# Kernel optimization log

Hardware: AMD Instinct MI355X
Metric: run time of the kernel (lower is better)

The kernel has to match this reference:

```python
import jax, jax.numpy as jnp
import numpy as np
from jax import lax

INPUT_SIZE, HIDDEN, NUM_LAYERS, NUM_CLASSES = 22, 10, 2, 4
B, T = 1024, 1000


def _run_layer(seq, w_ih, w_hh, b_ih, b_hh):
    # seq: (T, B, F_in) -> (T, B, H); Elman RNN with ReLU nonlinearity
    h0 = jnp.zeros((seq.shape[1], w_hh.shape[0]), seq.dtype)
    def step(h, x_t):
        h_new = jax.nn.relu(x_t @ w_ih.T + h @ w_hh.T + (b_ih + b_hh))
        return h_new, h_new
    _, hs = lax.scan(step, h0, seq)
    return hs


def setup_inputs() -> dict:
    key = jax.random.key(0)
    ks = jax.random.split(key, 12)
    s = 1.0 / np.sqrt(HIDDEN)  # torch nn.RNN init scale
    u = lambda k, shape: jax.random.uniform(k, shape, jnp.float32, -s, s)
    return {
        "x": jax.random.normal(ks[0], (B, T, INPUT_SIZE), jnp.float32),
        "w_ih0": u(ks[1], (HIDDEN, INPUT_SIZE)),
        "w_hh0": u(ks[2], (HIDDEN, HIDDEN)),
        "b_ih0": u(ks[3], (HIDDEN,)),
        "b_hh0": u(ks[4], (HIDDEN,)),
        "w_ih1": u(ks[5], (HIDDEN, HIDDEN)),
        "w_hh1": u(ks[6], (HIDDEN, HIDDEN)),
        "b_ih1": u(ks[7], (HIDDEN,)),
        "b_hh1": u(ks[8], (HIDDEN,)),
        "w_lin": u(ks[9], (NUM_CLASSES, HIDDEN)),
        "b_lin": u(ks[10], (NUM_CLASSES,)),
    }


def reference(x, w_ih0, w_hh0, b_ih0, b_hh0, w_ih1, w_hh1, b_ih1, b_hh1, w_lin, b_lin):
    seq = jnp.transpose(x, (1, 0, 2))                      # (T, B, F)
    h1 = _run_layer(seq, w_ih0, w_hh0, b_ih0, b_hh0)       # (T, B, H)
    h2 = _run_layer(h1, w_ih1, w_hh1, b_ih1, b_hh1)        # (T, B, H)
    last = jax.nn.relu(h2[-1])                             # (B, H)
    return last @ w_lin.T + b_lin                          # (B, num_classes)
```

## Files before the change

kernel.cpp:

```cpp
#include <hip/hip_runtime.h>

typedef float v2f __attribute__((ext_vector_type(2)));

namespace {

constexpr int Tn = 1000, Fn = 22, Hn = 10, Cn = 4;
constexpr int ROWB = Tn * Fn * 4;
constexpr int CHF  = 32 * Fn;
constexpr int CHB  = CHF * 4;

__device__ __forceinline__ v2f mk2(float a, float b) { v2f r; r.x=a; r.y=b; return r; }
__device__ __forceinline__ v2f fma2(v2f a, v2f b, v2f c) { return __builtin_elementwise_fma(a,b,c); }
__device__ __forceinline__ float rlane(float v, int l) {
    return __uint_as_float(__builtin_amdgcn_readlane(__float_as_uint(v), l));
}
__device__ __forceinline__ void gld_lds4(const float* g, float* l) {
    __builtin_amdgcn_global_load_lds(
        (const __attribute__((address_space(1))) unsigned int*)g,
        (__attribute__((address_space(3))) unsigned int*)l, 4, 0, 0);
}
__device__ __forceinline__ void sfence() { __builtin_amdgcn_sched_barrier(0); }

__global__ __launch_bounds__(64, 1) void rnn_fat2(
    const float* __restrict__ x,
    const float* __restrict__ w_ih0, const float* __restrict__ w_hh0,
    const float* __restrict__ b_ih0, const float* __restrict__ b_hh0,
    const float* __restrict__ w_ih1, const float* __restrict__ w_hh1,
    const float* __restrict__ b_ih1, const float* __restrict__ b_hh1,
    const float* __restrict__ w_lin, const float* __restrict__ b_lin,
    float* __restrict__ out)
{
    __shared__ __align__(16) float ch[2][CHF];

    const int lane = threadIdx.x;
    const int b    = blockIdx.x;
    const int half = lane >> 5;
    const int l31  = lane & 31;

    const int jz = (l31 < Hn) ? l31 : 0;
    const bool isl2 = (l31 >= 16) && (l31 < 16 + Hn);
    const int j2 = isl2 ? (l31 - 16) : 0;

    const float* pwa = (l31 < 16) ? (w_hh0 + jz * Hn) : (w_ih1 + j2 * Hn);
    float wa[Hn], wb[Hn];
    #pragma unroll
    for (int k = 0; k < Hn; ++k) wa[k] = pwa[k];
    #pragma unroll
    for (int k = 0; k < Hn; ++k) wb[k] = isl2 ? w_hh1[j2 * Hn + k] : 0.f;
    v2f wih0p[11];
    #pragma unroll
    for (int p = 0; p < 11; ++p)
        wih0p[p] = mk2(w_ih0[jz * Fn + 2*p], w_ih0[jz * Fn + 2*p + 1]);
    const float bias1  = b_ih0[jz] + b_hh0[jz];
    const float bias2v = b_ih1[j2] + b_hh1[j2];
    const v2f bz2 = mk2(bias1, 0.f);

    const bool mL = (lane < Hn);
    const bool mU = (lane >= 32) && (lane < 32+Hn);

    const float* __restrict__ xrow = x + (size_t)b * (Tn * Fn);

    auto stage = [&](int c) {
        float* dst = ch[c & 1];
        const float* src = xrow + c * CHF;
        if (c < 31) {
            #pragma unroll
            for (int k = 0; k < 11; ++k) gld_lds4(src + k*64 + lane, dst + k*64);
        } else {
            gld_lds4(src + lane, dst);
            gld_lds4(src + 64 + lane, dst + 64);
            if (lane < 48) gld_lds4(src + 128 + lane, dst + 128);
        }
    };
    stage(0); stage(1);

    v2f xd[11], xv0[11], xv1[11];
    {
        const float* r01 = xrow + half * Fn;
        #pragma unroll
        for (int p = 0; p < 11; ++p) xd[p] = ((const v2f*)r01)[p];
        const float* r23 = xrow + (2 + half) * Fn;
        #pragma unroll
        for (int p = 0; p < 11; ++p) xv0[p] = ((const v2f*)r23)[p];
    }

    auto zc = [&](const v2f* xp) -> float {
        v2f z = fma2(xp[0], wih0p[0], bz2);
        #pragma unroll
        for (int p = 1; p < 11; ++p) z = fma2(xp[p], wih0p[p], z);
        return z.x + z.y;
    };

    auto pairptr = [&](int P) -> const float* {
        return &ch[(P >> 4) & 1][(P & 15) * 44 + half * 22];
    };
    auto loadxv = [&](v2f* dst, const float* rp) {
        #pragma unroll
        for (int p = 0; p < 11; ++p) dst[p] = ((const v2f*)rp)[p];
        sfence();
    };

    float S1[Hn], S2[Hn];
    #pragma unroll
    for (int k = 0; k < Hn; ++k) { S1[k] = 0.f; S2[k] = 0.f; }

    asm volatile("s_waitcnt vmcnt(0)" ::: "memory");
    float zA = zc(xd);
    float zB;

    auto dostep = [&](bool up, float z, bool commit2) {
        const float base = (up ? mU : mL) ? z : bias2v;
        float a = fmaf(S1[0], wa[0], base);
        float c = S1[1] * wa[1];
        a = fmaf(S1[2], wa[2], a);  c = fmaf(S1[3], wa[3], c);
        a = fmaf(S1[4], wa[4], a);  c = fmaf(S1[5], wa[5], c);
        a = fmaf(S1[6], wa[6], a);  c = fmaf(S1[7], wa[7], c);
        a = fmaf(S1[8], wa[8], a);  c = fmaf(S1[9], wa[9], c);
        a = fmaf(S2[0], wb[0], a);  c = fmaf(S2[1], wb[1], c);
        a = fmaf(S2[2], wb[2], a);  c = fmaf(S2[3], wb[3], c);
        a = fmaf(S2[4], wb[4], a);  c = fmaf(S2[5], wb[5], c);
        a = fmaf(S2[6], wb[6], a);  c = fmaf(S2[7], wb[7], c);
        a = fmaf(S2[8], wb[8], a);  c = fmaf(S2[9], wb[9], c);
        const float hn = fmaxf(a + c, 0.f);
        if (!up) {
            #pragma unroll
            for (int k = 0; k < Hn; ++k) S1[k] = rlane(hn, k);
            if (commit2) {
                #pragma unroll
                for (int k = 0; k < Hn; ++k) S2[k] = rlane(hn, 16 + k);
            }
        } else {
            #pragma unroll
            for (int k = 0; k < Hn; ++k) S1[k] = rlane(hn, 32 + k);
            if (commit2) {
                #pragma unroll
                for (int k = 0; k < Hn; ++k) S2[k] = rlane(hn, 48 + k);
            }
        }
    };

    auto MACRO = [&](int m, bool s2_0, bool ld0, bool ld1, bool z1) {
        if (ld0) loadxv(xv1, pairptr(2*m + 2));
        dostep(false, zA, s2_0);
        zB = zc(xv0);
        dostep(true, zA, true);
        if (ld1) loadxv(xv0, pairptr(2*m + 3));
        dostep(false, zB, true);
        if (z1) zA = zc(xv1);
        dostep(true, zB, true);
    };

    MACRO(0, false, true, true, true);

    #pragma unroll 1
    for (int m = 1; m < 249; ++m) {
        if ((m & 7) == 7) {
            asm volatile("s_waitcnt vmcnt(0)" ::: "memory");
            const int c = (m >> 3) + 2;
            if (c <= 31) stage(c);
        }
        MACRO(m, true, true, true, true);
    }
    MACRO(249, true, false, false, false);

    {
        float a = fmaf(S1[0], wa[0], bias2v);
        float c = S1[1] * wa[1];
        a = fmaf(S1[2], wa[2], a);  c = fmaf(S1[3], wa[3], c);
        a = fmaf(S1[4], wa[4], a);  c = fmaf(S1[5], wa[5], c);
        a = fmaf(S1[6], wa[6], a);  c = fmaf(S1[7], wa[7], c);
        a = fmaf(S1[8], wa[8], a);  c = fmaf(S1[9], wa[9], c);
        a = fmaf(S2[0], wb[0], a);  c = fmaf(S2[1], wb[1], c);
        a = fmaf(S2[2], wb[2], a);  c = fmaf(S2[3], wb[3], c);
        a = fmaf(S2[4], wb[4], a);  c = fmaf(S2[5], wb[5], c);
        a = fmaf(S2[6], wb[6], a);  c = fmaf(S2[7], wb[7], c);
        a = fmaf(S2[8], wb[8], a);  c = fmaf(S2[9], wb[9], c);
        const float hn = fmaxf(a + c, 0.f);
        #pragma unroll
        for (int k = 0; k < Hn; ++k) S2[k] = rlane(hn, 16 + k);
    }

    const int jc = (lane < Cn) ? lane : 0;
    float o = b_lin[jc];
    #pragma unroll
    for (int k = 0; k < Hn; ++k) o = fmaf(S2[k], w_lin[jc * Hn + k], o);
    if (lane < Cn) out[b * Cn + lane] = o;
}

}

extern "C" void kernel_launch(void* const* d_in, const int* in_sizes, int n_in,
                              void* d_out, int out_size, void* d_ws, size_t ws_size,
                              hipStream_t stream) {
    const float* x     = (const float*)d_in[0];
    const float* w_ih0 = (const float*)d_in[1];
    const float* w_hh0 = (const float*)d_in[2];
    const float* b_ih0 = (const float*)d_in[3];
    const float* b_hh0 = (const float*)d_in[4];
    const float* w_ih1 = (const float*)d_in[5];
    const float* w_hh1 = (const float*)d_in[6];
    const float* b_ih1 = (const float*)d_in[7];
    const float* b_hh1 = (const float*)d_in[8];
    const float* w_lin = (const float*)d_in[9];
    const float* b_lin = (const float*)d_in[10];
    float* out = (float*)d_out;

    rnn_fat2<<<dim3(1024), dim3(64), 0, stream>>>(
        x, w_ih0, w_hh0, b_ih0, b_hh0,
        w_ih1, w_hh1, b_ih1, b_hh1, w_lin, b_lin, out);
}
```

Baseline: 116.7 us.

## Split RNN layers across two wavefronts with an LDS ring pipeline

Replaces the single-wave kernel, which computed both layers in one interleaved dependency chain, with a two-wave block. Wave 0 runs layer 0 and writes hidden states into a double-buffered LDS ring. Wave 1 consumes them 32 timesteps behind to run layer 1 and the final linear layer. Each wave now has a shorter serial chain per step (10 FMAs instead of 20 for layer 0), at the cost of LDS traffic, a block barrier every 32 steps, and twice as many waves per CU.

```diff
diff --git a/kernel.cpp b/kernel.cpp
--- a/kernel.cpp
+++ b/kernel.cpp
@@ -5,9 +5,9 @@
 namespace {
 
 constexpr int Tn = 1000, Fn = 22, Hn = 10, Cn = 4;
-constexpr int ROWB = Tn * Fn * 4;
-constexpr int CHF  = 32 * Fn;
-constexpr int CHB  = CHF * 4;
+constexpr int CHF   = 32 * Fn;
+constexpr int RINGF = 2 * CHF;
+constexpr int LDSF  = RINGF + 2 * 32 * 16;
 
 __device__ __forceinline__ v2f mk2(float a, float b) { v2f r; r.x=a; r.y=b; return r; }
 __device__ __forceinline__ v2f fma2(v2f a, v2f b, v2f c) { return __builtin_elementwise_fma(a,b,c); }
@@ -20,8 +20,12 @@
         (__attribute__((address_space(3))) unsigned int*)l, 4, 0, 0);
 }
 __device__ __forceinline__ void sfence() { __builtin_amdgcn_sched_barrier(0); }
-
-__global__ __launch_bounds__(64, 1) void rnn_fat2(
+__device__ __forceinline__ void lgkm0_bar() {
+    asm volatile("s_waitcnt lgkmcnt(0)" ::: "memory");
+    __builtin_amdgcn_s_barrier();
+}
+
+__global__ __launch_bounds__(128, 2) void rnn_pipe(
     const float* __restrict__ x,
     const float* __restrict__ w_ih0, const float* __restrict__ w_hh0,
     const float* __restrict__ b_ih0, const float* __restrict__ b_hh0,
@@ -30,161 +34,202 @@
     const float* __restrict__ w_lin, const float* __restrict__ b_lin,
     float* __restrict__ out)
 {
-    __shared__ __align__(16) float ch[2][CHF];
-
-    const int lane = threadIdx.x;
+    __shared__ __align__(16) float lds[LDSF];
+    float* xch  = lds;
+    float* ring = lds + RINGF;
+
+    const int tid  = threadIdx.x;
+    const int wid  = tid >> 6;
+    const int lane = tid & 63;
     const int b    = blockIdx.x;
-    const int half = lane >> 5;
-    const int l31  = lane & 31;
-
-    const int jz = (l31 < Hn) ? l31 : 0;
-    const bool isl2 = (l31 >= 16) && (l31 < 16 + Hn);
-    const int j2 = isl2 ? (l31 - 16) : 0;
-
-    const float* pwa = (l31 < 16) ? (w_hh0 + jz * Hn) : (w_ih1 + j2 * Hn);
-    float wa[Hn], wb[Hn];
-    #pragma unroll
-    for (int k = 0; k < Hn; ++k) wa[k] = pwa[k];
-    #pragma unroll
-    for (int k = 0; k < Hn; ++k) wb[k] = isl2 ? w_hh1[j2 * Hn + k] : 0.f;
-    v2f wih0p[11];
-    #pragma unroll
-    for (int p = 0; p < 11; ++p)
-        wih0p[p] = mk2(w_ih0[jz * Fn + 2*p], w_ih0[jz * Fn + 2*p + 1]);
-    const float bias1  = b_ih0[jz] + b_hh0[jz];
-    const float bias2v = b_ih1[j2] + b_hh1[j2];
-    const v2f bz2 = mk2(bias1, 0.f);
-
-    const bool mL = (lane < Hn);
-    const bool mU = (lane >= 32) && (lane < 32+Hn);
-
     const float* __restrict__ xrow = x + (size_t)b * (Tn * Fn);
 
-    auto stage = [&](int c) {
-        float* dst = ch[c & 1];
-        const float* src = xrow + c * CHF;
-        if (c < 31) {
-            #pragma unroll
-            for (int k = 0; k < 11; ++k) gld_lds4(src + k*64 + lane, dst + k*64);
-        } else {
-            gld_lds4(src + lane, dst);
-            gld_lds4(src + 64 + lane, dst + 64);
-            if (lane < 48) gld_lds4(src + 128 + lane, dst + 128);
+    if (wid == 0) {
+        const int half = lane >> 5;
+        const int l31  = lane & 31;
+        const int jz   = (l31 < Hn) ? l31 : 0;
+
+        v2f wih0p[11];
+        #pragma unroll
+        for (int p = 0; p < 11; ++p)
+            wih0p[p] = mk2(w_ih0[jz*Fn + 2*p], w_ih0[jz*Fn + 2*p + 1]);
+        float wa[Hn];
+        #pragma unroll
+        for (int k = 0; k < Hn; ++k) wa[k] = w_hh0[jz*Hn + k];
+        const v2f bz2 = mk2(b_ih0[jz] + b_hh0[jz], 0.f);
+
+        const int jslotE = (lane < 10) ? lane : 10;
+        const int jslotO = (lane >= 32 && lane < 42) ? (lane - 32) : 11;
+
+        auto stage = [&](int c) {
+            float* dst = xch + (c & 1) * CHF;
+            const float* src = xrow + c * CHF;
+            if (c < 31) {
+                #pragma unroll
+                for (int k = 0; k < 11; ++k) gld_lds4(src + k*64 + lane, dst + k*64);
+            } else {
+                gld_lds4(src + lane, dst);
+                gld_lds4(src + 64 + lane, dst + 64);
+                if (lane < 48) gld_lds4(src + 128 + lane, dst + 128);
+            }
+        };
+
+        v2f xv0[11], xv1[11];
+        float S1[Hn];
+        #pragma unroll
+        for (int k = 0; k < Hn; ++k) S1[k] = 0.f;
+
+        auto zc = [&](const v2f* xp) -> float {
+            v2f z = fma2(xp[0], wih0p[0], bz2);
+            #pragma unroll
+            for (int p = 1; p < 11; ++p) z = fma2(xp[p], wih0p[p], z);
+            return z.x + z.y;
+        };
+        auto loadxv = [&](v2f* dst, const float* rp) {
+            #pragma unroll
+            for (int p = 0; p < 11; ++p) dst[p] = *(const v2f*)(rp + 2*p);
+            sfence();
+        };
+
+        float zA, zB;
+        auto aStep = [&](bool up, float z, float* wptr, int foff) {
+            float a = fmaf(S1[0], wa[0], z);
+            float c = S1[1]*wa[1];
+            a = fmaf(S1[2],wa[2],a);  c = fmaf(S1[3],wa[3],c);
+            a = fmaf(S1[4],wa[4],a);  c = fmaf(S1[5],wa[5],c);
+            a = fmaf(S1[6],wa[6],a);  c = fmaf(S1[7],wa[7],c);
+            a = fmaf(S1[8],wa[8],a);  c = fmaf(S1[9],wa[9],c);
+            const float hn = fmaxf(a + c, 0.f);
+            const int base = up ? 32 : 0;
+            #pragma unroll
+            for (int k = 0; k < Hn; ++k) S1[k] = rlane(hn, base + k);
+            wptr[foff] = hn;
+        };
+        auto aMacro = [&](const float* xb_t, const float* xb_n, int mm,
+                          float* wE, float* wO, bool ld0, bool ld1, bool z1) {
+            const float* l0 = (mm < 7) ? xb_t + (2*mm + 2)*44 : xb_n;
+            const float* l1 = (mm < 7) ? xb_t + (2*mm + 3)*44 : xb_n + 44;
+            if (ld0) loadxv(xv1, l0);
+            aStep(false, zA, wE, mm*64);
+            zB = zc(xv0);
+            aStep(true,  zA, wO, mm*64 + 16);
+            if (ld1) loadxv(xv0, l1);
+            aStep(false, zB, wE, mm*64 + 32);
+            if (z1) zA = zc(xv1);
+            aStep(true,  zB, wO, mm*64 + 48);
+        };
+
+        stage(0); stage(1);
+        {
+            v2f xd[11];
+            const float* r01 = xrow + half * Fn;
+            #pragma unroll
+            for (int p = 0; p < 11; ++p) xd[p] = *(const v2f*)(r01 + 2*p);
+            const float* r23 = xrow + (2 + half) * Fn;
+            #pragma unroll
+            for (int p = 0; p < 11; ++p) xv0[p] = *(const v2f*)(r23 + 2*p);
+            asm volatile("s_waitcnt vmcnt(0)" ::: "memory");
+            zA = zc(xd);
         }
-    };
-    stage(0); stage(1);
-
-    v2f xd[11], xv0[11], xv1[11];
-    {
-        const float* r01 = xrow + half * Fn;
-        #pragma unroll
-        for (int p = 0; p < 11; ++p) xd[p] = ((const v2f*)r01)[p];
-        const float* r23 = xrow + (2 + half) * Fn;
-        #pragma unroll
-        for (int p = 0; p < 11; ++p) xv0[p] = ((const v2f*)r23)[p];
+
+        #pragma unroll 1
+        for (int p = 0; p <= 32; ++p) {
+            if (p <= 30) {
+                const int xs = p & 1;
+                const float* xb_t = xch + xs*CHF + half*22;
+                const float* xb_n = xch + (xs^1)*CHF + half*22;
+                float* wE = ring + xs*512 + jslotE;
+                float* wO = ring + xs*512 + jslotO;
+                #pragma unroll
+                for (int mm = 0; mm < 7; ++mm)
+                    aMacro(xb_t, xb_n, mm, wE, wO, true, true, true);
+                asm volatile("s_waitcnt vmcnt(0)" ::: "memory");
+                if (p <= 29) stage(p + 2);
+                aMacro(xb_t, xb_n, 7, wE, wO, true, true, true);
+            } else if (p == 31) {
+                const float* xb_t = xch + CHF + half*22;
+                const float* xb_n = xch + half*22;
+                float* wE = ring + 512 + jslotE;
+                float* wO = ring + 512 + jslotO;
+                aMacro(xb_t, xb_n, 0, wE, wO, true, true, true);
+                aMacro(xb_t, xb_n, 1, wE, wO, false, false, false);
+            }
+            lgkm0_bar();
+        }
+    } else {
+        const int j2 = (lane < Hn) ? lane : 0;
+        v2f wih1p[5];
+        #pragma unroll
+        for (int p = 0; p < 5; ++p)
+            wih1p[p] = mk2(w_ih1[j2*Hn + 2*p], w_ih1[j2*Hn + 2*p + 1]);
+        float whh1r[Hn];
+        #pragma unroll
+        for (int k = 0; k < Hn; ++k) whh1r[k] = w_hh1[j2*Hn + k];
+        const v2f b2v = mk2(b_ih1[j2] + b_hh1[j2], 0.f);
+        const int jc = (lane < Cn) ? lane : 0;
+        float wl[Hn];
+        #pragma unroll
+        for (int k = 0; k < Hn; ++k) wl[k] = w_lin[jc*Hn + k];
+        const float blv = b_lin[jc];
+
+        float S2[Hn];
+        #pragma unroll
+        for (int k = 0; k < Hn; ++k) S2[k] = 0.f;
+        v2f hv0[5], hv1[5];
+
+        auto bload = [&](v2f* d, const float* rp) {
+            #pragma unroll
+            for (int k = 0; k < 5; ++k) d[k] = *(const v2f*)(rp + 2*k);
+            sfence();
+        };
+        auto bStep = [&](const v2f* hp) {
+            v2f acc = fma2(hp[0], wih1p[0], b2v);
+            acc = fma2(hp[1], wih1p[1], acc);
+            acc = fma2(hp[2], wih1p[2], acc);
+            acc = fma2(hp[3], wih1p[3], acc);
+            acc = fma2(hp[4], wih1p[4], acc);
+            float d = acc.x + acc.y;
+            d = fmaf(S2[0],whh1r[0],d);  d = fmaf(S2[1],whh1r[1],d);
+            d = fmaf(S2[2],whh1r[2],d);  d = fmaf(S2[3],whh1r[3],d);
+            d = fmaf(S2[4],whh1r[4],d);  d = fmaf(S2[5],whh1r[5],d);
+            d = fmaf(S2[6],whh1r[6],d);  d = fmaf(S2[7],whh1r[7],d);
+            d = fmaf(S2[8],whh1r[8],d);  d = fmaf(S2[9],whh1r[9],d);
+            const float hn = fmaxf(d, 0.f);
+            #pragma unroll
+            for (int k = 0; k < Hn; ++k) S2[k] = rlane(hn, k);
+        };
+
+        #pragma unroll 1
+        for (int p = 0; p <= 32; ++p) {
+            if (p >= 1) {
+                const float* rb = ring + ((p-1) & 1) * 512;
+                bload(hv0, rb);
+                if (p < 32) {
+                    #pragma unroll
+                    for (int s = 0; s < 32; ++s) {
+                        v2f* cur = (s & 1) ? hv1 : hv0;
+                        v2f* nxt = (s & 1) ? hv0 : hv1;
+                        if (s + 1 < 32) bload(nxt, rb + (s+1)*16);
+                        bStep(cur);
+                    }
+                } else {
+                    #pragma unroll
+                    for (int s = 0; s < 8; ++s) {
+                        v2f* cur = (s & 1) ? hv1 : hv0;
+                        v2f* nxt = (s & 1) ? hv0 : hv1;
+                        if (s + 1 < 8) bload(nxt, rb + (s+1)*16);
+                        bStep(cur);
+                    }
+                }
+            }
+            lgkm0_bar();
+        }
+
+        float o = blv;
+        #pragma unroll
+        for (int k = 0; k < Hn; ++k) o = fmaf(S2[k], wl[k], o);
+        if (lane < Cn) out[b * Cn + lane] = o;
     }
-
-    auto zc = [&](const v2f* xp) -> float {
-        v2f z = fma2(xp[0], wih0p[0], bz2);
-        #pragma unroll
-        for (int p = 1; p < 11; ++p) z = fma2(xp[p], wih0p[p], z);
-        return z.x + z.y;
-    };
-
-    auto pairptr = [&](int P) -> const float* {
-        return &ch[(P >> 4) & 1][(P & 15) * 44 + half * 22];
-    };
-    auto loadxv = [&](v2f* dst, const float* rp) {
-        #pragma unroll
-        for (int p = 0; p < 11; ++p) dst[p] = ((const v2f*)rp)[p];
-        sfence();
-    };
-
-    float S1[Hn], S2[Hn];
-    #pragma unroll
-    for (int k = 0; k < Hn; ++k) { S1[k] = 0.f; S2[k] = 0.f; }
-
-    asm volatile("s_waitcnt vmcnt(0)" ::: "memory");
-    float zA = zc(xd);
-    float zB;
-
-    auto dostep = [&](bool up, float z, bool commit2) {
-        const float base = (up ? mU : mL) ? z : bias2v;
-        float a = fmaf(S1[0], wa[0], base);
-        float c = S1[1] * wa[1];
-        a = fmaf(S1[2], wa[2], a);  c = fmaf(S1[3], wa[3], c);
-        a = fmaf(S1[4], wa[4], a);  c = fmaf(S1[5], wa[5], c);
-        a = fmaf(S1[6], wa[6], a);  c = fmaf(S1[7], wa[7], c);
-        a = fmaf(S1[8], wa[8], a);  c = fmaf(S1[9], wa[9], c);
-        a = fmaf(S2[0], wb[0], a);  c = fmaf(S2[1], wb[1], c);
-        a = fmaf(S2[2], wb[2], a);  c = fmaf(S2[3], wb[3], c);
-        a = fmaf(S2[4], wb[4], a);  c = fmaf(S2[5], wb[5], c);
-        a = fmaf(S2[6], wb[6], a);  c = fmaf(S2[7], wb[7], c);
-        a = fmaf(S2[8], wb[8], a);  c = fmaf(S2[9], wb[9], c);
-        const float hn = fmaxf(a + c, 0.f);
-        if (!up) {
-            #pragma unroll
-            for (int k = 0; k < Hn; ++k) S1[k] = rlane(hn, k);
-            if (commit2) {
-                #pragma unroll
-                for (int k = 0; k < Hn; ++k) S2[k] = rlane(hn, 16 + k);
-            }
-        } else {
-            #pragma unroll
-            for (int k = 0; k < Hn; ++k) S1[k] = rlane(hn, 32 + k);
-            if (commit2) {
-                #pragma unroll
-                for (int k = 0; k < Hn; ++k) S2[k] = rlane(hn, 48 + k);
-            }
-        }
-    };
-
-    auto MACRO = [&](int m, bool s2_0, bool ld0, bool ld1, bool z1) {
-        if (ld0) loadxv(xv1, pairptr(2*m + 2));
-        dostep(false, zA, s2_0);
-        zB = zc(xv0);
-        dostep(true, zA, true);
-        if (ld1) loadxv(xv0, pairptr(2*m + 3));
-        dostep(false, zB, true);
-        if (z1) zA = zc(xv1);
-        dostep(true, zB, true);
-    };
-
-    MACRO(0, false, true, true, true);
-
-    #pragma unroll 1
-    for (int m = 1; m < 249; ++m) {
-        if ((m & 7) == 7) {
-            asm volatile("s_waitcnt vmcnt(0)" ::: "memory");
-            const int c = (m >> 3) + 2;
-            if (c <= 31) stage(c);
-        }
-        MACRO(m, true, true, true, true);
-    }
-    MACRO(249, true, false, false, false);
-
-    {
-        float a = fmaf(S1[0], wa[0], bias2v);
-        float c = S1[1] * wa[1];
-        a = fmaf(S1[2], wa[2], a);  c = fmaf(S1[3], wa[3], c);
-        a = fmaf(S1[4], wa[4], a);  c = fmaf(S1[5], wa[5], c);
-        a = fmaf(S1[6], wa[6], a);  c = fmaf(S1[7], wa[7], c);
-        a = fmaf(S1[8], wa[8], a);  c = fmaf(S1[9], wa[9], c);
-        a = fmaf(S2[0], wb[0], a);  c = fmaf(S2[1], wb[1], c);
-        a = fmaf(S2[2], wb[2], a);  c = fmaf(S2[3], wb[3], c);
-        a = fmaf(S2[4], wb[4], a);  c = fmaf(S2[5], wb[5], c);
-        a = fmaf(S2[6], wb[6], a);  c = fmaf(S2[7], wb[7], c);
-        a = fmaf(S2[8], wb[8], a);  c = fmaf(S2[9], wb[9], c);
-        const float hn = fmaxf(a + c, 0.f);
-        #pragma unroll
-        for (int k = 0; k < Hn; ++k) S2[k] = rlane(hn, 16 + k);
-    }
-
-    const int jc = (lane < Cn) ? lane : 0;
-    float o = b_lin[jc];
-    #pragma unroll
-    for (int k = 0; k < Hn; ++k) o = fmaf(S2[k], w_lin[jc * Hn + k], o);
-    if (lane < Cn) out[b * Cn + lane] = o;
 }
 
 }
@@ -205,7 +250,7 @@
     const float* b_lin = (const float*)d_in[10];
     float* out = (float*)d_out;
 
-    rnn_fat2<<<dim3(1024), dim3(64), 0, stream>>>(
+    rnn_pipe<<<dim3(1024), dim3(128), 0, stream>>>(
         x, w_ih0, w_hh0, b_ih0, b_hh0,
         w_ih1, w_hh1, b_ih1, b_hh1, w_lin, b_lin, out);
 }
```

Result: slower. 137.3 us (+17.6%).

## Exchange hidden state through LDS broadcast instead of readlane

Applied to the files above, without the earlier changes.

Replaces the per-step v_readlane broadcast of the hidden state, which took 20 scalar readlanes per step, with writes of each lane's output into a small LDS scratch area followed by broadcast v2f reads. The recurrent dot products now use packed v2f FMAs with split accumulators for layer 1 and layer 2. The aim is to shorten the serial per-timestep critical path. The trade-off is LDS write-to-read latency on every step, and it depends on ordering within a single wave without explicit waits.

```diff
diff --git a/kernel.cpp b/kernel.cpp
--- a/kernel.cpp
+++ b/kernel.cpp
@@ -5,23 +5,24 @@
 namespace {
 
 constexpr int Tn = 1000, Fn = 22, Hn = 10, Cn = 4;
-constexpr int ROWB = Tn * Fn * 4;
 constexpr int CHF  = 32 * Fn;
-constexpr int CHB  = CHF * 4;
-
-__device__ __forceinline__ v2f mk2(float a, float b) { v2f r; r.x=a; r.y=b; return r; }
-__device__ __forceinline__ v2f fma2(v2f a, v2f b, v2f c) { return __builtin_elementwise_fma(a,b,c); }
-__device__ __forceinline__ float rlane(float v, int l) {
+constexpr int HB   = 2 * CHF;
+constexpr int LDSF = HB + 128;
+
+__device__ __forceinline__ v2f mk2(float a, float b){ v2f r; r.x=a; r.y=b; return r; }
+__device__ __forceinline__ v2f fma2(v2f a, v2f b, v2f c){ return __builtin_elementwise_fma(a,b,c); }
+__device__ __forceinline__ float rlane(float v, int l){
     return __uint_as_float(__builtin_amdgcn_readlane(__float_as_uint(v), l));
 }
-__device__ __forceinline__ void gld_lds4(const float* g, float* l) {
+__device__ __forceinline__ void gld_lds4(const float* g, float* l){
     __builtin_amdgcn_global_load_lds(
         (const __attribute__((address_space(1))) unsigned int*)g,
         (__attribute__((address_space(3))) unsigned int*)l, 4, 0, 0);
 }
-__device__ __forceinline__ void sfence() { __builtin_amdgcn_sched_barrier(0); }
-
-__global__ __launch_bounds__(64, 1) void rnn_fat2(
+__device__ __forceinline__ void sfence(){ __builtin_amdgcn_sched_barrier(0); }
+
+
+__global__ __launch_bounds__(64, 1) void rnn_lds(
     const float* __restrict__ x,
     const float* __restrict__ w_ih0, const float* __restrict__ w_hh0,
     const float* __restrict__ b_ih0, const float* __restrict__ b_hh0,
@@ -30,38 +31,40 @@
     const float* __restrict__ w_lin, const float* __restrict__ b_lin,
     float* __restrict__ out)
 {
-    __shared__ __align__(16) float ch[2][CHF];
+    __shared__ __align__(16) float lds[LDSF];
 
     const int lane = threadIdx.x;
     const int b    = blockIdx.x;
     const int half = lane >> 5;
     const int l31  = lane & 31;
-
-    const int jz = (l31 < Hn) ? l31 : 0;
-    const bool isl2 = (l31 >= 16) && (l31 < 16 + Hn);
-    const int j2 = isl2 ? (l31 - 16) : 0;
-
-    const float* pwa = (l31 < 16) ? (w_hh0 + jz * Hn) : (w_ih1 + j2 * Hn);
-    float wa[Hn], wb[Hn];
-    #pragma unroll
-    for (int k = 0; k < Hn; ++k) wa[k] = pwa[k];
-    #pragma unroll
-    for (int k = 0; k < Hn; ++k) wb[k] = isl2 ? w_hh1[j2 * Hn + k] : 0.f;
-    v2f wih0p[11];
+    const int jz   = (l31 < Hn) ? l31 : 0;
+    const int j2   = (l31 >= 16 && l31 < 16 + Hn) ? (l31 - 16) : 0;
+    const bool isH1 = (l31 < 16);
+
+    v2f wih0p[11], whh0p[5], wih1p[5], whh1p[5];
     #pragma unroll
     for (int p = 0; p < 11; ++p)
-        wih0p[p] = mk2(w_ih0[jz * Fn + 2*p], w_ih0[jz * Fn + 2*p + 1]);
-    const float bias1  = b_ih0[jz] + b_hh0[jz];
-    const float bias2v = b_ih1[j2] + b_hh1[j2];
-    const v2f bz2 = mk2(bias1, 0.f);
-
-    const bool mL = (lane < Hn);
-    const bool mU = (lane >= 32) && (lane < 32+Hn);
+        wih0p[p] = mk2(w_ih0[jz*Fn + 2*p], w_ih0[jz*Fn + 2*p + 1]);
+    #pragma unroll
+    for (int k = 0; k < 5; ++k) {
+        whh0p[k] = mk2(w_hh0[jz*Hn + 2*k], w_hh0[jz*Hn + 2*k + 1]);
+        wih1p[k] = mk2(w_ih1[j2*Hn + 2*k], w_ih1[j2*Hn + 2*k + 1]);
+        whh1p[k] = mk2(w_hh1[j2*Hn + 2*k], w_hh1[j2*Hn + 2*k + 1]);
+    }
+    const v2f bz2 = mk2(b_ih0[jz] + b_hh0[jz], 0.f);
+    const v2f b2p = mk2(b_ih1[j2] + b_hh1[j2], 0.f);
+
+    const int dmp = HB + 64 + lane;
+    float* pwE  = lds + ((lane < 10) ? HB + lane
+                        : (lane >= 16 && lane < 26) ? HB + 48 + (lane - 16) : dmp);
+    float* pwO  = lds + ((lane >= 32 && lane < 42) ? HB + 16 + (lane - 32)
+                        : (lane >= 48 && lane < 58) ? HB + 32 + (lane - 48) : dmp);
+    float* pwE0 = lds + ((lane < 10) ? HB + lane : dmp);
 
     const float* __restrict__ xrow = x + (size_t)b * (Tn * Fn);
 
-    auto stage = [&](int c) {
-        float* dst = ch[c & 1];
+    auto stage = [&](int c){
+        float* dst = lds + (c & 1) * CHF;
         const float* src = xrow + c * CHF;
         if (c < 31) {
             #pragma unroll
@@ -72,86 +75,100 @@
             if (lane < 48) gld_lds4(src + 128 + lane, dst + 128);
         }
     };
+
+    lds[HB + lane] = 0.f;
+    lds[HB + 64 + lane] = 0.f;
+
     stage(0); stage(1);
 
-    v2f xd[11], xv0[11], xv1[11];
+    v2f xv0[11], xv1[11];
     {
         const float* r01 = xrow + half * Fn;
         #pragma unroll
-        for (int p = 0; p < 11; ++p) xd[p] = ((const v2f*)r01)[p];
+        for (int p = 0; p < 11; ++p) xv1[p] = *(const v2f*)(r01 + 2*p);
         const float* r23 = xrow + (2 + half) * Fn;
         #pragma unroll
-        for (int p = 0; p < 11; ++p) xv0[p] = ((const v2f*)r23)[p];
-    }
-
-    auto zc = [&](const v2f* xp) -> float {
+        for (int p = 0; p < 11; ++p) xv0[p] = *(const v2f*)(r23 + 2*p);
+    }
+
+    auto zc = [&](const v2f* xp)->float{
         v2f z = fma2(xp[0], wih0p[0], bz2);
         #pragma unroll
         for (int p = 1; p < 11; ++p) z = fma2(xp[p], wih0p[p], z);
         return z.x + z.y;
     };
-
-    auto pairptr = [&](int P) -> const float* {
-        return &ch[(P >> 4) & 1][(P & 15) * 44 + half * 22];
-    };
-    auto loadxv = [&](v2f* dst, const float* rp) {
-        #pragma unroll
-        for (int p = 0; p < 11; ++p) dst[p] = ((const v2f*)rp)[p];
+    auto pairptr = [&](int P)->const float*{
+        return lds + ((P >> 4) & 1) * CHF + (P & 15) * 44 + half * 22;
+    };
+    auto loadxv = [&](v2f* dst, const float* rp){
+        #pragma unroll
+        for (int p = 0; p < 11; ++p) dst[p] = *(const v2f*)(rp + 2*p);
         sfence();
     };
 
-    float S1[Hn], S2[Hn];
-    #pragma unroll
-    for (int k = 0; k < Hn; ++k) { S1[k] = 0.f; S2[k] = 0.f; }
-
+    v2f h1a[5], h2a[5], h1b[5], h2b[5];
+    auto readE = [&](v2f* d1, v2f* d2){
+        #pragma unroll
+        for (int k = 0; k < 5; ++k) d1[k] = *(const v2f*)&lds[HB + 16 + 2*k];
+        #pragma unroll
+        for (int k = 0; k < 5; ++k) d2[k] = *(const v2f*)&lds[HB + 32 + 2*k];
+        sfence();
+    };
+    auto readO = [&](v2f* d1, v2f* d2){
+        #pragma unroll
+        for (int k = 0; k < 5; ++k) d1[k] = *(const v2f*)&lds[HB + 0 + 2*k];
+        #pragma unroll
+        for (int k = 0; k < 5; ++k) d2[k] = *(const v2f*)&lds[HB + 48 + 2*k];
+        sfence();
+    };
+
+    auto core = [&](float z, const v2f* c1, const v2f* c2)->float{
+        v2f A = c1[0] * whh0p[0];
+        A = fma2(c1[1], whh0p[1], A);
+        A = fma2(c1[2], whh0p[2], A);
+        A = fma2(c1[3], whh0p[3], A);
+        A = fma2(c1[4], whh0p[4], A);
+        v2f B = fma2(c1[0], wih1p[0], b2p);
+        B = fma2(c1[1], wih1p[1], B);
+        B = fma2(c1[2], wih1p[2], B);
+        B = fma2(c1[3], wih1p[3], B);
+        B = fma2(c1[4], wih1p[4], B);
+        B = fma2(c2[0], whh1p[0], B);
+        B = fma2(c2[1], whh1p[1], B);
+        B = fma2(c2[2], whh1p[2], B);
+        B = fma2(c2[3], whh1p[3], B);
+        B = fma2(c2[4], whh1p[4], B);
+        const float a1s = (A.x + A.y) + z;
+        const float a2s = B.x + B.y;
+        return fmaxf(isH1 ? a1s : a2s, 0.f);
+    };
+
+    float zA, zB;
     asm volatile("s_waitcnt vmcnt(0)" ::: "memory");
-    float zA = zc(xd);
-    float zB;
-
-    auto dostep = [&](bool up, float z, bool commit2) {
-        const float base = (up ? mU : mL) ? z : bias2v;
-        float a = fmaf(S1[0], wa[0], base);
-        float c = S1[1] * wa[1];
-        a = fmaf(S1[2], wa[2], a);  c = fmaf(S1[3], wa[3], c);
-        a = fmaf(S1[4], wa[4], a);  c = fmaf(S1[5], wa[5], c);
-        a = fmaf(S1[6], wa[6], a);  c = fmaf(S1[7], wa[7], c);
-        a = fmaf(S1[8], wa[8], a);  c = fmaf(S1[9], wa[9], c);
-        a = fmaf(S2[0], wb[0], a);  c = fmaf(S2[1], wb[1], c);
-        a = fmaf(S2[2], wb[2], a);  c = fmaf(S2[3], wb[3], c);
-        a = fmaf(S2[4], wb[4], a);  c = fmaf(S2[5], wb[5], c);
-        a = fmaf(S2[6], wb[6], a);  c = fmaf(S2[7], wb[7], c);
-        a = fmaf(S2[8], wb[8], a);  c = fmaf(S2[9], wb[9], c);
-        const float hn = fmaxf(a + c, 0.f);
-        if (!up) {
-            #pragma unroll
-            for (int k = 0; k < Hn; ++k) S1[k] = rlane(hn, k);
-            if (commit2) {
-                #pragma unroll
-                for (int k = 0; k < Hn; ++k) S2[k] = rlane(hn, 16 + k);
-            }
-        } else {
-            #pragma unroll
-            for (int k = 0; k < Hn; ++k) S1[k] = rlane(hn, 32 + k);
-            if (commit2) {
-                #pragma unroll
-                for (int k = 0; k < Hn; ++k) S2[k] = rlane(hn, 48 + k);
-            }
-        }
-    };
-
-    auto MACRO = [&](int m, bool s2_0, bool ld0, bool ld1, bool z1) {
+    zA = zc(xv1);
+
+    readE(h1a, h2a);
+
+    auto MACRO = [&](int m, float* pwEf, bool ld0, bool ld1, bool zA1){
+        float hn = core(zA, h1a, h2a);
+        *pwEf = hn;
+        readO(h1b, h2b);
         if (ld0) loadxv(xv1, pairptr(2*m + 2));
-        dostep(false, zA, s2_0);
+        hn = core(zA, h1b, h2b);
+        *pwO = hn;
+        readE(h1a, h2a);
         zB = zc(xv0);
-        dostep(true, zA, true);
+        hn = core(zB, h1a, h2a);
+        *pwE = hn;
+        readO(h1b, h2b);
         if (ld1) loadxv(xv0, pairptr(2*m + 3));
-        dostep(false, zB, true);
-        if (z1) zA = zc(xv1);
-        dostep(true, zB, true);
-    };
-
-    MACRO(0, false, true, true, true);
-
+        hn = core(zB, h1b, h2b);
+        *pwO = hn;
+        readE(h1a, h2a);
+        if (zA1) zA = zc(xv1);
+    };
+
+    MACRO(0, pwE0, true, true, true);
     #pragma unroll 1
     for (int m = 1; m < 249; ++m) {
         if ((m & 7) == 7) {
@@ -159,31 +176,31 @@
             const int c = (m >> 3) + 2;
             if (c <= 31) stage(c);
         }
-        MACRO(m, true, true, true, true);
-    }
-    MACRO(249, true, false, false, false);
-
+        MACRO(m, pwE, true, true, true);
+    }
+    MACRO(249, pwE, false, false, false);
+
+    float S2[Hn];
     {
-        float a = fmaf(S1[0], wa[0], bias2v);
-        float c = S1[1] * wa[1];
-        a = fmaf(S1[2], wa[2], a);  c = fmaf(S1[3], wa[3], c);
-        a = fmaf(S1[4], wa[4], a);  c = fmaf(S1[5], wa[5], c);
-        a = fmaf(S1[6], wa[6], a);  c = fmaf(S1[7], wa[7], c);
-        a = fmaf(S1[8], wa[8], a);  c = fmaf(S1[9], wa[9], c);
-        a = fmaf(S2[0], wb[0], a);  c = fmaf(S2[1], wb[1], c);
-        a = fmaf(S2[2], wb[2], a);  c = fmaf(S2[3], wb[3], c);
-        a = fmaf(S2[4], wb[4], a);  c = fmaf(S2[5], wb[5], c);
-        a = fmaf(S2[6], wb[6], a);  c = fmaf(S2[7], wb[7], c);
-        a = fmaf(S2[8], wb[8], a);  c = fmaf(S2[9], wb[9], c);
-        const float hn = fmaxf(a + c, 0.f);
-        #pragma unroll
-        for (int k = 0; k < Hn; ++k) S2[k] = rlane(hn, 16 + k);
+        v2f B = fma2(h1a[0], wih1p[0], b2p);
+        B = fma2(h1a[1], wih1p[1], B);
+        B = fma2(h1a[2], wih1p[2], B);
+        B = fma2(h1a[3], wih1p[3], B);
+        B = fma2(h1a[4], wih1p[4], B);
+        B = fma2(h2a[0], whh1p[0], B);
+        B = fma2(h2a[1], whh1p[1], B);
+        B = fma2(h2a[2], whh1p[2], B);
+        B = fma2(h2a[3], whh1p[3], B);
+        B = fma2(h2a[4], whh1p[4], B);
+        const float h2f = fmaxf(B.x + B.y, 0.f);
+        #pragma unroll
+        for (int k = 0; k < Hn; ++k) S2[k] = rlane(h2f, 16 + k);
     }
 
     const int jc = (lane < Cn) ? lane : 0;
     float o = b_lin[jc];
     #pragma unroll
-    for (int k = 0; k < Hn; ++k) o = fmaf(S2[k], w_lin[jc * Hn + k], o);
+    for (int k = 0; k < Hn; ++k) o = fmaf(S2[k], w_lin[jc*Hn + k], o);
     if (lane < Cn) out[b * Cn + lane] = o;
 }
 
@@ -205,7 +222,7 @@
     const float* b_lin = (const float*)d_in[10];
     float* out = (float*)d_out;
 
-    rnn_fat2<<<dim3(1024), dim3(64), 0, stream>>>(
+    rnn_lds<<<dim3(1024), dim3(64), 0, stream>>>(
         x, w_ih0, w_hh0, b_ih0, b_hh0,
         w_ih1, w_hh1, b_ih1, b_hh1, w_lin, b_lin, out);
 }
```

New measurement: 142.8 us. 22.4% more time.

## Pack hidden state to fp16 pairs and use fdot2 for recurrent matvec

Applied to the files above, without the earlier changes.

Hidden states and recurrent weights are stored as packed fp16 pairs, and the recurrence uses v_dot2 instructions that accumulate in fp32. The state broadcast needs half as many readlanes, since a DPP swap plus cvt_pkrtz packs neighbouring lanes into one register first. This shortens the serial per-step critical path of FMAs and readlanes. In exchange, state and weights lose precision to fp16 rounding over 1000 recurrent steps, which risks accuracy drift.

```diff
diff --git a/kernel.cpp b/kernel.cpp
--- a/kernel.cpp
+++ b/kernel.cpp
@@ -1,27 +1,30 @@
 #include <hip/hip_runtime.h>
 
 typedef float v2f __attribute__((ext_vector_type(2)));
+typedef _Float16 h2f __attribute__((ext_vector_type(2)));
 
 namespace {
 
 constexpr int Tn = 1000, Fn = 22, Hn = 10, Cn = 4;
-constexpr int ROWB = Tn * Fn * 4;
-constexpr int CHF  = 32 * Fn;
-constexpr int CHB  = CHF * 4;
-
-__device__ __forceinline__ v2f mk2(float a, float b) { v2f r; r.x=a; r.y=b; return r; }
-__device__ __forceinline__ v2f fma2(v2f a, v2f b, v2f c) { return __builtin_elementwise_fma(a,b,c); }
-__device__ __forceinline__ float rlane(float v, int l) {
+constexpr int CHF = 32 * Fn;
+
+__device__ __forceinline__ v2f mk2(float a, float b){ v2f r; r.x=a; r.y=b; return r; }
+__device__ __forceinline__ v2f fma2(v2f a, v2f b, v2f c){ return __builtin_elementwise_fma(a,b,c); }
+__device__ __forceinline__ float rlanef(float v, int l){
     return __uint_as_float(__builtin_amdgcn_readlane(__float_as_uint(v), l));
 }
-__device__ __forceinline__ void gld_lds4(const float* g, float* l) {
+__device__ __forceinline__ unsigned rlaneu(unsigned v, int l){
+    return (unsigned)__builtin_amdgcn_readlane((int)v, l);
+}
+__device__ __forceinline__ void gld_lds4(const float* g, float* l){
     __builtin_amdgcn_global_load_lds(
         (const __attribute__((address_space(1))) unsigned int*)g,
         (__attribute__((address_space(3))) unsigned int*)l, 4, 0, 0);
 }
-__device__ __forceinline__ void sfence() { __builtin_amdgcn_sched_barrier(0); }
-
-__global__ __launch_bounds__(64, 1) void rnn_fat2(
+__device__ __forceinline__ void sfence(){ __builtin_amdgcn_sched_barrier(0); }
+__device__ __forceinline__ h2f u2h(unsigned u){ return __builtin_bit_cast(h2f, u); }
+
+__global__ __launch_bounds__(64, 1) void rnn_dot16(
     const float* __restrict__ x,
     const float* __restrict__ w_ih0, const float* __restrict__ w_hh0,
     const float* __restrict__ b_ih0, const float* __restrict__ b_hh0,
@@ -42,15 +45,19 @@
     const int j2 = isl2 ? (l31 - 16) : 0;
 
     const float* pwa = (l31 < 16) ? (w_hh0 + jz * Hn) : (w_ih1 + j2 * Hn);
-    float wa[Hn], wb[Hn];
-    #pragma unroll
-    for (int k = 0; k < Hn; ++k) wa[k] = pwa[k];
-    #pragma unroll
-    for (int k = 0; k < Hn; ++k) wb[k] = isl2 ? w_hh1[j2 * Hn + k] : 0.f;
+    h2f waH[5], wbH[5];
+    #pragma unroll
+    for (int k = 0; k < 5; ++k) {
+        h2f t; t.x = (_Float16)pwa[2*k]; t.y = (_Float16)pwa[2*k+1];
+        waH[k] = t;
+        h2f u; u.x = isl2 ? (_Float16)w_hh1[j2*Hn + 2*k]     : (_Float16)0.f;
+               u.y = isl2 ? (_Float16)w_hh1[j2*Hn + 2*k + 1] : (_Float16)0.f;
+        wbH[k] = u;
+    }
     v2f wih0p[11];
     #pragma unroll
     for (int p = 0; p < 11; ++p)
-        wih0p[p] = mk2(w_ih0[jz * Fn + 2*p], w_ih0[jz * Fn + 2*p + 1]);
+        wih0p[p] = mk2(w_ih0[jz*Fn + 2*p], w_ih0[jz*Fn + 2*p + 1]);
     const float bias1  = b_ih0[jz] + b_hh0[jz];
     const float bias2v = b_ih1[j2] + b_hh1[j2];
     const v2f bz2 = mk2(bias1, 0.f);
@@ -78,10 +85,10 @@
     {
         const float* r01 = xrow + half * Fn;
         #pragma unroll
-        for (int p = 0; p < 11; ++p) xd[p] = ((const v2f*)r01)[p];
+        for (int p = 0; p < 11; ++p) xd[p] = *(const v2f*)(r01 + 2*p);
         const float* r23 = xrow + (2 + half) * Fn;
         #pragma unroll
-        for (int p = 0; p < 11; ++p) xv0[p] = ((const v2f*)r23)[p];
+        for (int p = 0; p < 11; ++p) xv0[p] = *(const v2f*)(r23 + 2*p);
     }
 
     auto zc = [&](const v2f* xp) -> float {
@@ -90,52 +97,43 @@
         for (int p = 1; p < 11; ++p) z = fma2(xp[p], wih0p[p], z);
         return z.x + z.y;
     };
-
     auto pairptr = [&](int P) -> const float* {
         return &ch[(P >> 4) & 1][(P & 15) * 44 + half * 22];
     };
     auto loadxv = [&](v2f* dst, const float* rp) {
         #pragma unroll
-        for (int p = 0; p < 11; ++p) dst[p] = ((const v2f*)rp)[p];
+        for (int p = 0; p < 11; ++p) dst[p] = *(const v2f*)(rp + 2*p);
         sfence();
     };
 
-    float S1[Hn], S2[Hn];
-    #pragma unroll
-    for (int k = 0; k < Hn; ++k) { S1[k] = 0.f; S2[k] = 0.f; }
-
+    unsigned S1u[5], S2u[5];
+    #pragma unroll
+    for (int k = 0; k < 5; ++k) { S1u[k] = 0u; S2u[k] = 0u; }
+
+    float zA, zB;
     asm volatile("s_waitcnt vmcnt(0)" ::: "memory");
-    float zA = zc(xd);
-    float zB;
+    zA = zc(xd);
 
     auto dostep = [&](bool up, float z, bool commit2) {
         const float base = (up ? mU : mL) ? z : bias2v;
-        float a = fmaf(S1[0], wa[0], base);
-        float c = S1[1] * wa[1];
-        a = fmaf(S1[2], wa[2], a);  c = fmaf(S1[3], wa[3], c);
-        a = fmaf(S1[4], wa[4], a);  c = fmaf(S1[5], wa[5], c);
-        a = fmaf(S1[6], wa[6], a);  c = fmaf(S1[7], wa[7], c);
-        a = fmaf(S1[8], wa[8], a);  c = fmaf(S1[9], wa[9], c);
-        a = fmaf(S2[0], wb[0], a);  c = fmaf(S2[1], wb[1], c);
-        a = fmaf(S2[2], wb[2], a);  c = fmaf(S2[3], wb[3], c);
-        a = fmaf(S2[4], wb[4], a);  c = fmaf(S2[5], wb[5], c);
-        a = fmaf(S2[6], wb[6], a);  c = fmaf(S2[7], wb[7], c);
-        a = fmaf(S2[8], wb[8], a);  c = fmaf(S2[9], wb[9], c);
-        const float hn = fmaxf(a + c, 0.f);
-        if (!up) {
+        float aA = base, aB = 0.f;
+        #pragma unroll
+        for (int k = 0; k < 5; ++k)
+            aA = __builtin_amdgcn_fdot2(u2h(S1u[k]), waH[k], aA, false);
+        #pragma unroll
+        for (int k = 0; k < 5; ++k)
+            aB = __builtin_amdgcn_fdot2(u2h(S2u[k]), wbH[k], aB, false);
+        const float hn = fmaxf(aA + aB, 0.f);
+        const float nb = __uint_as_float((unsigned)__builtin_amdgcn_mov_dpp(
+                             (int)__float_as_uint(hn), 0xB1, 0xF, 0xF, false));
+        const unsigned pk = __builtin_bit_cast(unsigned,
+                             __builtin_amdgcn_cvt_pkrtz(hn, nb));
+        const int s1b = up ? 32 : 0;
+        #pragma unroll
+        for (int k = 0; k < 5; ++k) S1u[k] = rlaneu(pk, s1b + 2*k);
+        if (commit2) {
             #pragma unroll
-            for (int k = 0; k < Hn; ++k) S1[k] = rlane(hn, k);
-            if (commit2) {
-                #pragma unroll
-                for (int k = 0; k < Hn; ++k) S2[k] = rlane(hn, 16 + k);
-            }
-        } else {
-            #pragma unroll
-            for (int k = 0; k < Hn; ++k) S1[k] = rlane(hn, 32 + k);
-            if (commit2) {
-                #pragma unroll
-                for (int k = 0; k < Hn; ++k) S2[k] = rlane(hn, 48 + k);
-            }
+            for (int k = 0; k < 5; ++k) S2u[k] = rlaneu(pk, s1b + 16 + 2*k);
         }
     };
 
@@ -163,27 +161,24 @@
     }
     MACRO(249, true, false, false, false);
 
+    float S2f[Hn];
     {
-        float a = fmaf(S1[0], wa[0], bias2v);
-        float c = S1[1] * wa[1];
-        a = fmaf(S1[2], wa[2], a);  c = fmaf(S1[3], wa[3], c);
-        a = fmaf(S1[4], wa[4], a);  c = fmaf(S1[5], wa[5], c);
-        a = fmaf(S1[6], wa[6], a);  c = fmaf(S1[7], wa[7], c);
-        a = fmaf(S1[8], wa[8], a);  c = fmaf(S1[9], wa[9], c);
-        a = fmaf(S2[0], wb[0], a);  c = fmaf(S2[1], wb[1], c);
-        a = fmaf(S2[2], wb[2], a);  c = fmaf(S2[3], wb[3], c);
-        a = fmaf(S2[4], wb[4], a);  c = fmaf(S2[5], wb[5], c);
-        a = fmaf(S2[6], wb[6], a);  c = fmaf(S2[7], wb[7], c);
-        a = fmaf(S2[8], wb[8], a);  c = fmaf(S2[9], wb[9], c);
-        const float hn = fmaxf(a + c, 0.f);
-        #pragma unroll
-        for (int k = 0; k < Hn; ++k) S2[k] = rlane(hn, 16 + k);
+        float aA = bias2v, aB = 0.f;
+        #pragma unroll
+        for (int k = 0; k < 5; ++k)
+            aA = __builtin_amdgcn_fdot2(u2h(S1u[k]), waH[k], aA, false);
+        #pragma unroll
+        for (int k = 0; k < 5; ++k)
+            aB = __builtin_amdgcn_fdot2(u2h(S2u[k]), wbH[k], aB, false);
+        const float h2f_ = fmaxf(aA + aB, 0.f);
+        #pragma unroll
+        for (int k = 0; k < Hn; ++k) S2f[k] = rlanef(h2f_, 16 + k);
     }
 
     const int jc = (lane < Cn) ? lane : 0;
     float o = b_lin[jc];
     #pragma unroll
-    for (int k = 0; k < Hn; ++k) o = fmaf(S2[k], w_lin[jc * Hn + k], o);
+    for (int k = 0; k < Hn; ++k) o = fmaf(S2f[k], w_lin[jc*Hn + k], o);
     if (lane < Cn) out[b * Cn + lane] = o;
 }
 
@@ -205,7 +200,7 @@
     const float* b_lin = (const float*)d_in[10];
     float* out = (float*)d_out;
 
-    rnn_fat2<<<dim3(1024), dim3(64), 0, stream>>>(
+    rnn_dot16<<<dim3(1024), dim3(64), 0, stream>>>(
         x, w_ih0, w_hh0, b_ih0, b_hh0,
         w_ih1, w_hh1, b_ih1, b_hh1, w_lin, b_lin, out);
 }
```

After: 104.0 us. 10.9% less time.
